# Kernel tuning notes

Measured on AMD Instinct MI355X. Metric: run time of the kernel, lower is better.

## Reference

```python
import jax, jax.numpy as jnp
import numpy as np

N = 100000      # num nodes
M = 25000       # num hyperedges
E = 600000      # num incidences (node, hyperedge) pairs
D_IN, D_HID, D_OUT = 128, 128, 128


def setup_inputs() -> dict:
    key = jax.random.key(0)
    ks = jax.random.split(key, 9)
    s_in = 1.0 / np.sqrt(D_IN)
    s_hid = 1.0 / np.sqrt(D_HID)
    return {
        "x": jax.random.normal(ks[0], (N, D_IN), dtype=jnp.float32),
        "W1": jax.random.normal(ks[1], (D_IN, D_HID), dtype=jnp.float32) * s_in,
        "b1": jnp.zeros((D_HID,), dtype=jnp.float32),
        "W2": jax.random.normal(ks[2], (D_HID, D_HID), dtype=jnp.float32) * s_hid,
        "b2": jnp.zeros((D_HID,), dtype=jnp.float32),
        "W3": jax.random.normal(ks[3], (D_HID, D_OUT), dtype=jnp.float32) * s_hid,
        "b3": jnp.zeros((D_OUT,), dtype=jnp.float32),
        "node_idx": jax.random.randint(ks[4], (E,), 0, N, dtype=jnp.int32),
        "hedge_idx": jax.random.randint(ks[5], (E,), 0, M, dtype=jnp.int32),
        "num_hyperedges": M,
    }


def _hypergraph_conv(x, W, b, node_idx, hedge_idx, num_hyperedges):
    """PyG HypergraphConv (use_attention=False, hyperedge_weight=1):
    out = D^-1 H B^-1 H^T (x @ W) + b
    """
    n = x.shape[0]
    x = x @ W                                   # [N, F_out]
    ones = jnp.ones(node_idx.shape[0], dtype=x.dtype)
    deg_n = jax.ops.segment_sum(ones, node_idx, num_segments=n)              # D
    deg_e = jax.ops.segment_sum(ones, hedge_idx, num_segments=num_hyperedges)  # B
    d_inv = jnp.where(deg_n > 0, 1.0 / deg_n, 0.0)
    b_inv = jnp.where(deg_e > 0, 1.0 / deg_e, 0.0)
    # node -> hyperedge: m_e = B^-1 sum_{i in e} x_i
    m = jax.ops.segment_sum(x[node_idx], hedge_idx, num_segments=num_hyperedges)
    m = m * b_inv[:, None]
    # hyperedge -> node: out_i = D^-1 sum_{e ni i} m_e
    out = jax.ops.segment_sum(m[hedge_idx], node_idx, num_segments=n)
    out = out * d_inv[:, None]
    return out + b


def reference(x, W1, b1, W2, b2, W3, b3, node_idx, hedge_idx, num_hyperedges):
    # dropout is identity in eval mode (training=False)
    x = jax.nn.elu(_hypergraph_conv(x, W1, b1, node_idx, hedge_idx, num_hyperedges))
    x = jax.nn.elu(_hypergraph_conv(x, W2, b2, node_idx, hedge_idx, num_hyperedges))
    x = jax.nn.elu(_hypergraph_conv(x, W3, b3, node_idx, hedge_idx, num_hyperedges))
    return x
```

## Files before the change

### kernel.cpp

```cpp
#include <hip/hip_runtime.h>

#define NN 100000
#define MM 25000
#define EE 600000
#define TT (MM + NN)

#define NB 782
#define CAP 2048
#define TILE_E 2048
#define GA ((EE + TILE_E - 1) / TILE_E)
#define CVT_B 1024
#define ND_BLOCKS 2048

typedef __attribute__((ext_vector_type(8))) short short8;
typedef __attribute__((ext_vector_type(4))) float floatx4;

__device__ __forceinline__ float bl(unsigned int u){ return __uint_as_float(u << 16); }
__device__ __forceinline__ float bh(unsigned int u){ return __uint_as_float(u & 0xffff0000u); }
__device__ __forceinline__ unsigned int packbf2(float a, float b){
    unsigned int ua = __float_as_uint(a), ub = __float_as_uint(b);
    ua = (ua + 0x7fffu + ((ua >> 16) & 1u)) >> 16;
    ub = (ub + 0x7fffu + ((ub >> 16) & 1u)) & 0xffff0000u;
    return ua | ub;
}
__device__ __forceinline__ unsigned short f2bf(float f){
    unsigned int u = __float_as_uint(f);
    return (unsigned short)((u + 0x7fffu + ((u >> 16) & 1u)) >> 16);
}
__device__ __forceinline__ void acc8(float* a, uint4 v){
    a[0] += bl(v.x); a[1] += bh(v.x);
    a[2] += bl(v.y); a[3] += bh(v.y);
    a[4] += bl(v.z); a[5] += bh(v.z);
    a[6] += bl(v.w); a[7] += bh(v.w);
}

__global__ __launch_bounds__(256) void k_fused(const float* __restrict__ x, unsigned int* __restrict__ xb,
                        const float* __restrict__ W1, const float* __restrict__ W2,
                        const float* __restrict__ W3, unsigned short* __restrict__ WT,
                        const int* __restrict__ nidx, const int* __restrict__ hidx,
                        int* __restrict__ gcur, unsigned int* __restrict__ items) {
    __shared__ int h[NB];
    __shared__ int cur[NB];
    int b = blockIdx.x;
    int t = threadIdx.x;
    if (b < GA) {
        for (int i = t; i < NB; i += 256) h[i] = 0;
        __syncthreads();
        int base = b * TILE_E;
        #pragma unroll
        for (int k = 0; k < TILE_E / 256; k++) {
            int e = base + k * 256 + t;
            if (e < EE) {
                atomicAdd(&h[hidx[e] >> 6], 1);
                atomicAdd(&h[391 + (nidx[e] >> 8)], 1);
            }
        }
        __syncthreads();
        for (int i = t; i < NB; i += 256) {
            int c = h[i];
            cur[i] = c ? (i * CAP + atomicAdd(&gcur[i], c)) : 0;
        }
        __syncthreads();
        #pragma unroll
        for (int k = 0; k < TILE_E / 256; k++) {
            int e = base + k * 256 + t;
            if (e < EE) {
                int hh = hidx[e], nn = nidx[e];
                int p1 = atomicAdd(&cur[hh >> 6], 1);
                items[p1] = ((unsigned)(hh & 63) << 17) | (unsigned)nn;
                int p2 = atomicAdd(&cur[391 + (nn >> 8)], 1);
                items[p2] = ((unsigned)(nn & 255) << 15) | (unsigned)hh;
            }
        }
    } else if (b < GA + CVT_B) {
        const int F4 = NN * 32;
        for (int u = (b - GA) * 1024; u < F4; u += CVT_B * 1024) {
            float4 v0 = ((const float4*)x)[u + t];
            float4 v1 = ((const float4*)x)[u + 256 + t];
            float4 v2 = ((const float4*)x)[u + 512 + t];
            float4 v3 = ((const float4*)x)[u + 768 + t];
            uint2 o0, o1, o2, o3;
            o0.x = packbf2(v0.x, v0.y); o0.y = packbf2(v0.z, v0.w);
            o1.x = packbf2(v1.x, v1.y); o1.y = packbf2(v1.z, v1.w);
            o2.x = packbf2(v2.x, v2.y); o2.y = packbf2(v2.z, v2.w);
            o3.x = packbf2(v3.x, v3.y); o3.y = packbf2(v3.z, v3.w);
            ((uint2*)xb)[u + t] = o0;
            ((uint2*)xb)[u + 256 + t] = o1;
            ((uint2*)xb)[u + 512 + t] = o2;
            ((uint2*)xb)[u + 768 + t] = o3;
        }
    } else {
        int l = b - GA - CVT_B;
        const float* W = l == 0 ? W1 : (l == 1 ? W2 : W3);
        unsigned short* T = WT + l * 16384;
        for (int i = t; i < 16384; i += 256) {
            int k = i >> 7, c = i & 127;
            T[c * 128 + k] = f2bf(W[k * 128 + c]);
        }
    }
}

__global__ __launch_bounds__(256) void k_passB(unsigned int* __restrict__ items,
                                               const int* __restrict__ gcur,
                                               int2* __restrict__ ptr2, float* __restrict__ inv,
                                               int* __restrict__ chist) {
    __shared__ unsigned int led[CAP];
    __shared__ unsigned int grp[CAP];
    __shared__ int bins[256], cur[256], tmp[256];
    __shared__ int chs[32];
    int b = blockIdx.x, t = threadIdx.x;
    int base = b * CAP, cnt = gcur[b];
    bool he = b < 391;
    int nbins = he ? 64 : 256;
    int keybase = he ? b * 64 : MM + (b - 391) * 256;
    int shift = he ? 17 : 15;
    unsigned int mask = he ? 0x1FFFFu : 0x7FFFu;
    int keylim = he ? MM : TT;

    for (int i = t; i < cnt; i += 256) led[i] = items[base + i];
    bins[t] = 0;
    if (t < 32) chs[t] = 0;
    __syncthreads();
    for (int i = t; i < cnt; i += 256) atomicAdd(&bins[led[i] >> shift], 1);
    __syncthreads();
    int v = (t < nbins) ? bins[t] : 0;
    tmp[t] = v;
    __syncthreads();
    for (int o = 1; o < 256; o <<= 1) {
        int u = (t >= o) ? tmp[t - o] : 0;
        __syncthreads();
        tmp[t] += u;
        __syncthreads();
    }
    int excl = tmp[t] - v;
    if (t < nbins) {
        int g = keybase + t;
        if (g < keylim) {
            ptr2[g] = make_int2(base + excl, v);
            inv[g] = v ? 1.f / (float)v : 0.f;
            int cls = min((v + 7) >> 3, 15);
            atomicAdd(&chs[cls + (he ? 0 : 16)], 1);
        }
        cur[t] = excl;
    }
    __syncthreads();
    for (int i = t; i < cnt; i += 256) {
        unsigned int it = led[i];
        int p = atomicAdd(&cur[it >> shift], 1);
        grp[p] = it & mask;
    }
    __syncthreads();
    for (int i = t; i < cnt; i += 256) items[base + i] = grp[i];
    if (t < 32 && chs[t]) atomicAdd(&chist[t], chs[t]);
}

#define SCAT_BLOCKS 128
__global__ __launch_bounds__(256) void k_scatter(const int2* __restrict__ ptr2,
                                                 const int* __restrict__ chist, int* __restrict__ ccur,
                                                 int* __restrict__ perm) {
    __shared__ int off[32];
    __shared__ int lh[32];
    __shared__ int lcur[32];
    int t = threadIdx.x;
    if (t < 32) {
        int side = t >> 4, c = t & 15;
        int s = 0;
        for (int k = 0; k < c; k++) s += chist[side * 16 + k];
        off[t] = s;
        lh[t] = 0;
    }
    __syncthreads();
    const int chunk = (TT + SCAT_BLOCKS - 1) / SCAT_BLOCKS;
    int beg = blockIdx.x * chunk;
    int end = min(beg + chunk, TT);
    for (int g = beg + t; g < end; g += 256) {
        int v = ptr2[g].y;
        int cls = min((v + 7) >> 3, 15);
        atomicAdd(&lh[(g < MM ? 0 : 16) + cls], 1);
    }
    __syncthreads();
    if (t < 32) {
        int c = lh[t];
        lcur[t] = c ? (off[t] + atomicAdd(&ccur[t], c)) : 0;
    }
    __syncthreads();
    for (int g = beg + t; g < end; g += 256) {
        int v = ptr2[g].y;
        int cls = min((v + 7) >> 3, 15);
        bool he = g < MM;
        int slot = atomicAdd(&lcur[(he ? 0 : 16) + cls], 1);
        perm[(he ? 0 : MM) + slot] = he ? g : (g - MM);
    }
}

__device__ __forceinline__ void gather_row8(const unsigned int* __restrict__ X,
                                            const unsigned int* __restrict__ adj,
                                            int beg, int deg, int ql, float* a) {
    if (deg <= 0) return;
    int end = beg + deg;
    int n[8];
    #pragma unroll
    for (int i = 0; i < 8; i++) n[i] = (beg + i < end) ? (int)adj[beg + i] : -1;
    for (int j = beg; j < end; j += 8) {
        int jn = j + 8;
        int m[8];
        #pragma unroll
        for (int i = 0; i < 8; i++) m[i] = (jn + i < end) ? (int)adj[jn + i] : -1;
        uint4 v[8];
        #pragma unroll
        for (int i = 0; i < 8; i++) {
            v[i] = make_uint4(0u, 0u, 0u, 0u);
            if (n[i] >= 0) v[i] = *((const uint4*)(X + (unsigned)n[i] * 64u) + ql);
        }
        #pragma unroll
        for (int i = 0; i < 8; i++) acc8(a, v[i]);
        #pragma unroll
        for (int i = 0; i < 8; i++) n[i] = m[i];
    }
}

__global__ __launch_bounds__(256) void k_hegemm(const unsigned int* __restrict__ X,
        const int2* __restrict__ ptr2, const unsigned int* __restrict__ adj,
        const float* __restrict__ b_inv, const unsigned short* __restrict__ WT,
        const int* __restrict__ hperm, unsigned short* __restrict__ C) {
    __shared__ unsigned int tile[16 * 68];
    __shared__ int prow[16];
    int t = threadIdx.x;
    int qidx = t >> 4, ql = t & 15;
    int r0 = blockIdx.x * 16;
    int r = r0 + qidx;
    float a[8] = {0.f,0.f,0.f,0.f,0.f,0.f,0.f,0.f};
    float sc = 0.f;
    if (r < MM) {
        int rt = hperm[r];
        if (ql == 0) prow[qidx] = rt;
        int2 pe = ptr2[rt];
        gather_row8(X, adj, pe.x, pe.y, ql, a);
        sc = b_inv[rt];
    } else if (ql == 0) {
        prow[qidx] = -1;
    }
    uint4 o;
    o.x = packbf2(a[0] * sc, a[1] * sc);
    o.y = packbf2(a[2] * sc, a[3] * sc);
    o.z = packbf2(a[4] * sc, a[5] * sc);
    o.w = packbf2(a[6] * sc, a[7] * sc);
    *((uint4*)(tile + qidx * 68 + ql * 4)) = o;
    __syncthreads();

    int wv = t >> 6, lane = t & 63;
    int mm = lane & 15, quad = lane >> 4;
    floatx4 acc0 = (floatx4){0.f,0.f,0.f,0.f}, acc1 = acc0;
    int c0 = wv * 2;
    #pragma unroll
    for (int q = 0; q < 4; q++) {
        short8 af = *reinterpret_cast<const short8*>((const short*)(tile + mm * 68) + q * 32 + quad * 8);
        short8 b0 = *reinterpret_cast<const short8*>(WT + (c0 * 16 + mm) * 128 + q * 32 + quad * 8);
        short8 b1 = *reinterpret_cast<const short8*>(WT + ((c0 + 1) * 16 + mm) * 128 + q * 32 + quad * 8);
        acc0 = __builtin_amdgcn_mfma_f32_16x16x32_bf16(af, b0, acc0, 0, 0, 0);
        acc1 = __builtin_amdgcn_mfma_f32_16x16x32_bf16(af, b1, acc1, 0, 0, 0);
    }
    #pragma unroll
    for (int rg = 0; rg < 4; rg++) {
        int rr = prow[quad * 4 + rg];
        if (rr >= 0) {
            C[rr * 128 + c0 * 16 + mm]       = f2bf(acc0[rg]);
            C[rr * 128 + (c0 + 1) * 16 + mm] = f2bf(acc1[rg]);
        }
    }
}

template<bool F32OUT>
__global__ __launch_bounds__(256) void k_gather_nd(const unsigned int* __restrict__ X,
        const int2* __restrict__ ptr2, const unsigned int* __restrict__ adj,
        const float* __restrict__ d_inv, const float* __restrict__ bias,
        const int* __restrict__ nperm, void* __restrict__ out) {
    int lane = threadIdx.x & 63, quad = lane >> 4, ql = lane & 15;
    int wave0 = (blockIdx.x * 256 + threadIdx.x) >> 6;
    const int NWAVES = ND_BLOCKS * 4;
    const float4* b4 = (const float4*)bias;
    float4 bA = b4[ql * 2], bB = b4[ql * 2 + 1];
    for (int rq = wave0; rq < NN / 4; rq += NWAVES) {
        int r = rq * 4 + quad;
        int rt = nperm[r];
        int2 pe = ptr2[rt];
        float a[8] = {0.f,0.f,0.f,0.f,0.f,0.f,0.f,0.f};
        gather_row8(X, adj, pe.x, pe.y, ql, a);
        float sc = d_inv[rt];
        float f[8];
        f[0] = a[0] * sc + bA.x; f[1] = a[1] * sc + bA.y;
        f[2] = a[2] * sc + bA.z; f[3] = a[3] * sc + bA.w;
        f[4] = a[4] * sc + bB.x; f[5] = a[5] * sc + bB.y;
        f[6] = a[6] * sc + bB.z; f[7] = a[7] * sc + bB.w;
        #pragma unroll
        for (int i = 0; i < 8; i++) f[i] = f[i] > 0.f ? f[i] : __expf(f[i]) - 1.f;
        if (F32OUT) {
            float* o = (float*)out + (unsigned)rt * 128u;
            ((float4*)o)[ql * 2]     = make_float4(f[0], f[1], f[2], f[3]);
            ((float4*)o)[ql * 2 + 1] = make_float4(f[4], f[5], f[6], f[7]);
        } else {
            uint4 o4;
            o4.x = packbf2(f[0], f[1]); o4.y = packbf2(f[2], f[3]);
            o4.z = packbf2(f[4], f[5]); o4.w = packbf2(f[6], f[7]);
            ((uint4*)((unsigned int*)out + (unsigned)rt * 64u))[ql] = o4;
        }
    }
}

extern "C" void kernel_launch(void* const* d_in, const int* in_sizes, int n_in,
                              void* d_out, int out_size, void* d_ws, size_t ws_size,
                              hipStream_t stream) {
    const float* x  = (const float*)d_in[0];
    const float* W1 = (const float*)d_in[1];
    const float* b1 = (const float*)d_in[2];
    const float* W2 = (const float*)d_in[3];
    const float* b2 = (const float*)d_in[4];
    const float* W3 = (const float*)d_in[5];
    const float* b3 = (const float*)d_in[6];
    const int* nidx = (const int*)d_in[7];
    const int* hidx = (const int*)d_in[8];

    char* ws = (char*)d_ws;
    size_t o = 0;
    auto alloc = [&](size_t b) -> char* { char* p = ws + o; o = (o + b + 255) & ~(size_t)255; return p; };
    int2*  ptr2  = (int2*)alloc((size_t)TT * 8);
    float* invq  = (float*)alloc(TT * 4);
    int*   gcur  = (int*)alloc((NB + 64) * 4);
    unsigned int* items = (unsigned int*)alloc((size_t)NB * CAP * 4);
    unsigned short* WT   = (unsigned short*)alloc(3 * 128 * 128 * 2);
    unsigned short* mbuf = (unsigned short*)alloc((size_t)MM * 128 * 2);
    int* perm = (int*)alloc((size_t)TT * 4);
    int* chist = gcur + NB;
    int* ccur  = chist + 32;

    unsigned int* xb   = (unsigned int*)d_out;
    unsigned int* bufA = (unsigned int*)d_out;
    unsigned int* bufB = (unsigned int*)d_out + (size_t)NN * 64;

    hipMemsetAsync(gcur, 0, (NB + 64) * 4, stream);
    k_fused<<<GA + CVT_B + 3, 256, 0, stream>>>(x, xb, W1, W2, W3, WT, nidx, hidx, gcur, items);
    k_passB<<<NB, 256, 0, stream>>>(items, gcur, ptr2, invq, chist);
    k_scatter<<<SCAT_BLOCKS, 256, 0, stream>>>(ptr2, chist, ccur, perm);

    const float* b_inv = invq;
    const float* d_inv = invq + MM;
    const int2* nptr2 = ptr2 + MM;
    const int* hperm = perm;
    const int* nperm = perm + MM;
    const int grid_hg = (MM + 15) / 16;
    const unsigned int* adj = items;

    k_hegemm<<<grid_hg, 256, 0, stream>>>(xb, ptr2, adj, b_inv, WT, hperm, mbuf);
    k_gather_nd<false><<<ND_BLOCKS, 256, 0, stream>>>((const unsigned int*)mbuf, nptr2, adj, d_inv, b1, nperm, (void*)bufA);
    k_hegemm<<<grid_hg, 256, 0, stream>>>(bufA, ptr2, adj, b_inv, WT + 16384, hperm, mbuf);
    k_gather_nd<false><<<ND_BLOCKS, 256, 0, stream>>>((const unsigned int*)mbuf, nptr2, adj, d_inv, b2, nperm, (void*)bufB);
    k_hegemm<<<grid_hg, 256, 0, stream>>>(bufB, ptr2, adj, b_inv, WT + 32768, hperm, mbuf);
    k_gather_nd<true ><<<ND_BLOCKS, 256, 0, stream>>>((const unsigned int*)mbuf, nptr2, adj, d_inv, b3, nperm, d_out);
}
```

Measured before the change: 337.3 us.

## Stage bucketed incidence items in shared memory before coalesced global scatter

The bucketing phase now does a block-local prefix scan over bucket counts, writes items into a shared-memory staging buffer ordered by bucket, and then copies them out in contiguous runs per bucket. Before, each thread scattered items directly to global memory at random bucket offsets. The goal is more coalesced global writes. In exchange it adds a 256-wide scan with many barriers and roughly 24KB of extra LDS per block, which may lower occupancy for the other block roles in the fused kernel.

```diff
diff --git a/kernel.cpp b/kernel.cpp
--- a/kernel.cpp
+++ b/kernel.cpp
@@ -39,14 +39,18 @@
                         const float* __restrict__ W3, unsigned short* __restrict__ WT,
                         const int* __restrict__ nidx, const int* __restrict__ hidx,
                         int* __restrict__ gcur, unsigned int* __restrict__ items) {
-    __shared__ int h[NB];
-    __shared__ int cur[NB];
+    __shared__ int h[1024];
+    __shared__ int st[1024];
+    __shared__ int tmp[256];
+    __shared__ unsigned int g[2 * TILE_E];
+    __shared__ unsigned short bk[2 * TILE_E];
     int b = blockIdx.x;
     int t = threadIdx.x;
     if (b < GA) {
-        for (int i = t; i < NB; i += 256) h[i] = 0;
-        __syncthreads();
         int base = b * TILE_E;
+        int ne = min(TILE_E, EE - base);
+        for (int i = t; i < 1024; i += 256) h[i] = 0;
+        __syncthreads();
         #pragma unroll
         for (int k = 0; k < TILE_E / 256; k++) {
             int e = base + k * 256 + t;
@@ -56,9 +60,28 @@
             }
         }
         __syncthreads();
+        int c4[4]; int ts = 0;
+        #pragma unroll
+        for (int j = 0; j < 4; j++) { c4[j] = h[4 * t + j]; ts += c4[j]; }
+        tmp[t] = ts;
+        __syncthreads();
+        for (int o = 1; o < 256; o <<= 1) {
+            int u = (t >= o) ? tmp[t - o] : 0;
+            __syncthreads();
+            tmp[t] += u;
+            __syncthreads();
+        }
+        int run = tmp[t] - ts;
+        #pragma unroll
+        for (int j = 0; j < 4; j++) { st[4 * t + j] = run; run += c4[j]; }
+        __syncthreads();
         for (int i = t; i < NB; i += 256) {
-            int c = h[i];
-            cur[i] = c ? (i * CAP + atomicAdd(&gcur[i], c)) : 0;
+            int c = h[i], s = st[i];
+            if (c) {
+                int gb = i * CAP + atomicAdd(&gcur[i], c);
+                st[i] = gb - s;
+            }
+            h[i] = s;
         }
         __syncthreads();
         #pragma unroll
@@ -66,11 +89,20 @@
             int e = base + k * 256 + t;
             if (e < EE) {
                 int hh = hidx[e], nn = nidx[e];
-                int p1 = atomicAdd(&cur[hh >> 6], 1);
-                items[p1] = ((unsigned)(hh & 63) << 17) | (unsigned)nn;
-                int p2 = atomicAdd(&cur[391 + (nn >> 8)], 1);
-                items[p2] = ((unsigned)(nn & 255) << 15) | (unsigned)hh;
+                int b1 = hh >> 6;
+                int p1 = atomicAdd(&h[b1], 1);
+                g[p1] = ((unsigned)(hh & 63) << 17) | (unsigned)nn;
+                bk[p1] = (unsigned short)b1;
+                int b2 = 391 + (nn >> 8);
+                int p2 = atomicAdd(&h[b2], 1);
+                g[p2] = ((unsigned)(nn & 255) << 15) | (unsigned)hh;
+                bk[p2] = (unsigned short)b2;
             }
+        }
+        __syncthreads();
+        int total = 2 * ne;
+        for (int p = t; p < total; p += 256) {
+            items[st[bk[p]] + p] = g[p];
         }
     } else if (b < GA + CVT_B) {
         const int F4 = NN * 32;
```

Measured after the change: 322.6 us. 4.4% less time.
